# Performance work log

Hardware: AMD Instinct MI355X
Metric: run time of the kernel (lower is better)

## Reference

```python
import jax, jax.numpy as jnp
import numpy as np

V, D, T_MAX, H, L = 96, 128, 64, 8, 4
HD = D // H          # 16
FF = 4 * D           # 512
B, T = 4096, 64
EPS = 1e-5


def setup_inputs() -> dict:
    key = jax.random.key(0)
    ks = jax.random.split(key, 24)
    n = jax.random.normal
    inp = {
        'idx': jax.random.randint(ks[0], (B, T), 0, V),
        'targets': jax.random.randint(ks[1], (B, T), 0, V),
        'tok_emb': n(ks[2], (V, D), jnp.float32) * 0.02,
        'pos_emb': n(ks[3], (T_MAX, D), jnp.float32) * 0.02,
        # per-layer stacked params; weight layout follows torch Linear [out, in]
        'Wq': n(ks[4], (L, D, D), jnp.float32) * (1.0 / np.sqrt(D)),
        'Wk': n(ks[5], (L, D, D), jnp.float32) * (1.0 / np.sqrt(D)),
        'Wv': n(ks[6], (L, D, D), jnp.float32) * (1.0 / np.sqrt(D)),
        'Wo': n(ks[7], (L, D, D), jnp.float32) * (1.0 / np.sqrt(D)),
        'bo': jnp.zeros((L, D), jnp.float32),
        'ln1_g': jnp.ones((L, D), jnp.float32),
        'ln1_b': jnp.zeros((L, D), jnp.float32),
        'ln2_g': jnp.ones((L, D), jnp.float32),
        'ln2_b': jnp.zeros((L, D), jnp.float32),
        'W1': n(ks[8], (L, FF, D), jnp.float32) * (1.0 / np.sqrt(D)),
        'b1': jnp.zeros((L, FF), jnp.float32),
        'W2': n(ks[9], (L, D, FF), jnp.float32) * (1.0 / np.sqrt(FF)),
        'b2': jnp.zeros((L, D), jnp.float32),
        'lnf_g': jnp.ones((D,), jnp.float32),
        'lnf_b': jnp.zeros((D,), jnp.float32),
        'lm_b': jnp.zeros((V,), jnp.float32),
    }
    return inp


def _layernorm(x, g, b):
    mu = jnp.mean(x, axis=-1, keepdims=True)
    var = jnp.mean(jnp.square(x - mu), axis=-1, keepdims=True)
    return (x - mu) * jax.lax.rsqrt(var + EPS) * g + b


def reference(idx, targets, tok_emb, pos_emb, Wq, Wk, Wv, Wo, bo,
              ln1_g, ln1_b, ln2_g, ln2_b, W1, b1, W2, b2,
              lnf_g, lnf_b, lm_b):
    Bc, Tc = idx.shape
    x = tok_emb[idx] + pos_emb[:Tc]                      # [B,T,D]
    causal = jnp.tril(jnp.ones((Tc, Tc), bool))
    scale = HD ** -0.5
    for l in range(L):  # small fixed layer count
        xn = _layernorm(x, ln1_g[l], ln1_b[l])
        # per-head Linears are blocks of a single [D,D] matmul
        q = (xn @ Wq[l].T).reshape(Bc, Tc, H, HD)
        k = (xn @ Wk[l].T).reshape(Bc, Tc, H, HD)
        v = (xn @ Wv[l].T).reshape(Bc, Tc, H, HD)
        wei = jnp.einsum('bqhd,bkhd->bhqk', q, k) * scale
        wei = jnp.where(causal, wei, -jnp.inf)
        wei = jax.nn.softmax(wei, axis=-1)               # dropout = identity (eval)
        att = jnp.einsum('bhqk,bkhd->bqhd', wei, v).reshape(Bc, Tc, D)
        x = x + att @ Wo[l].T + bo[l]
        xn = _layernorm(x, ln2_g[l], ln2_b[l])
        h = jax.nn.gelu(xn @ W1[l].T + b1[l], approximate=False)
        x = x + h @ W2[l].T + b2[l]
    x = _layernorm(x, lnf_g, lnf_b)
    logits = x @ tok_emb.T + lm_b                        # tied weights
    logits = logits.reshape(Bc * Tc, V)
    logp = jax.nn.log_softmax(logits, axis=-1)
    loss = -jnp.mean(jnp.take_along_axis(logp, targets.reshape(-1, 1), axis=-1))
    return logits, loss
```

## Files before the change

### kernel.cpp

```cpp
#include <hip/hip_runtime.h>
#include <hip/hip_bf16.h>
#include <math.h>

#define PREP_THR 512

typedef __attribute__((ext_vector_type(8))) short bf16x8;
typedef __attribute__((ext_vector_type(4))) short bf16x4;
typedef __attribute__((ext_vector_type(4))) float f32x4;

#define MFMA32(a, b, c) __builtin_amdgcn_mfma_f32_16x16x32_bf16((a), (b), (c), 0, 0, 0)

#if defined(__has_builtin)
#if __has_builtin(__builtin_amdgcn_mfma_f32_16x16x16bf16_1k)
#define HAVE_MFMA16 1
#endif
#endif
#ifdef HAVE_MFMA16
#define MFMA16(a, b, c) __builtin_amdgcn_mfma_f32_16x16x16bf16_1k((a), (b), (c), 0, 0, 0)
#else
__device__ __forceinline__ f32x4 mfma16_fb(bf16x4 a, bf16x4 b, f32x4 c) {
  asm volatile("s_nop 1\n\tv_mfma_f32_16x16x16_bf16 %0, %1, %2, %0\n\ts_nop 7\n\ts_nop 7"
               : "+v"(c) : "v"(a), "v"(b));
  return c;
}
#define MFMA16(a, b, c) mfma16_fb((a), (b), (c))
#endif

#define WS_EMB 0
#define WS_WQ  12288
#define WS_WK  (WS_WQ + 65536)
#define WS_WV  (WS_WK + 65536)
#define WS_WO  (WS_WV + 65536)
#define WS_W1  (WS_WO + 65536)
#define WS_W2  (WS_W1 + 262144)
#define WS_END (WS_W2 + 262144)

__device__ __forceinline__ short f2bf(float f) {
  union { __hip_bfloat16 h; unsigned short s; } u;
  u.h = __float2bfloat16(f);
  return (short)u.s;
}
__device__ __forceinline__ bf16x4 pk4(f32x4 v) {
  bf16x4 r;
  r[0] = f2bf(v[0]); r[1] = f2bf(v[1]); r[2] = f2bf(v[2]); r[3] = f2bf(v[3]);
  return r;
}
__device__ __forceinline__ float gelu1(float x) {
  float y = x * __builtin_fmaf(0.0356774081f, x * x, 0.7978845608f);
  return x * __builtin_amdgcn_rcpf(1.f + exp2f(-2.885390082f * y));
}

__global__ void prep_weights(const float* __restrict__ tok_emb,
                             const float* __restrict__ Wq, const float* __restrict__ Wk,
                             const float* __restrict__ Wv, const float* __restrict__ Wo,
                             const float* __restrict__ W1, const float* __restrict__ W2,
                             short* __restrict__ wsb) {
  int i = blockIdx.x * PREP_THR + threadIdx.x;
  if (i < 12288) {
    int n = i >> 7, k = i & 127;
    wsb[WS_EMB + (k >> 3) * 768 + n * 8 + (k & 7)] = f2bf(tok_emb[i]);
    return;
  }
  i -= 12288;
  if (i < 262144) {
    int tensor = i >> 16;
    int rem = i & 65535;
    int l = rem >> 14;
    int w = rem & 16383;
    int n = w >> 7, k = w & 127;
    const float* src = tensor == 0 ? Wq : tensor == 1 ? Wk : tensor == 2 ? Wv : Wo;
    wsb[WS_WQ + tensor * 65536 + l * 16384 + (k >> 3) * 1024 + n * 8 + (k & 7)] =
        f2bf(src[rem]);
    return;
  }
  i -= 262144;
  if (i < 262144) {
    int l = i >> 16;
    int w = i & 65535;
    int n = w >> 7, k = w & 127;
    wsb[WS_W1 + l * 65536 + (k >> 3) * 4096 + n * 8 + (k & 7)] = f2bf(W1[i]);
    return;
  }
  i -= 262144;
  if (i < 262144) {
    int l = i >> 16;
    int w = i & 65535;
    int n = w >> 9, k = w & 511;
    wsb[WS_W2 + l * 65536 + (k >> 3) * 1024 + n * 8 + (k & 7)] = f2bf(W2[i]);
  }
}

__global__ __launch_bounds__(256, 2)
void lm_forward(const int* __restrict__ idx, const int* __restrict__ targets,
                const float* __restrict__ tok_emb, const float* __restrict__ pos_emb,
                const float* __restrict__ bo, const float* __restrict__ ln1_g,
                const float* __restrict__ ln1_b, const float* __restrict__ ln2_g,
                const float* __restrict__ ln2_b, const float* __restrict__ b1,
                const float* __restrict__ b2, const float* __restrict__ lnf_g,
                const float* __restrict__ lnf_b, const float* __restrict__ lm_b,
                const short* __restrict__ wsb, float* __restrict__ out,
                float* __restrict__ loss_part) {
  __shared__ __align__(16) short sXn[64 * 136];
  __shared__ __align__(16) char region[33792];
  __shared__ __align__(16) float sPart[4 * 64 * 2];
  __shared__ float sRed[64];
  short* sAtt = (short*)region;
  short* sH = (short*)region;
  float* sL = (float*)region;

  const int b = blockIdx.x;
  const int tid = threadIdx.x;
  const int wave = tid >> 6;
  const int lane = tid & 63;
  const int lr = lane & 15;
  const int lg = lane >> 4;
  const f32x4 fz = {0.f, 0.f, 0.f, 0.f};
  const float KSC = 0.360673760f;

  f32x4 x[2][4];
#pragma unroll
  for (int cg = 0; cg < 2; ++cg)
#pragma unroll
    for (int n = 0; n < 4; ++n) {
      int t = 16 * n + lr;
      int dim = wave * 32 + cg * 16 + lg * 4;
      int tk = idx[b * 64 + t];
      x[cg][n] = *(const f32x4*)(tok_emb + tk * 128 + dim) +
                 *(const f32x4*)(pos_emb + t * 128 + dim);
    }

  auto ln = [&](const float* g, const float* be) {
    float s[4], s2[4];
#pragma unroll
    for (int n = 0; n < 4; ++n) {
      float a = 0.f, a2 = 0.f;
#pragma unroll
      for (int cg = 0; cg < 2; ++cg)
#pragma unroll
        for (int r = 0; r < 4; ++r) {
          float v = x[cg][n][r];
          a += v; a2 += v * v;
        }
      s[n] = a; s2[n] = a2;
    }
#pragma unroll
    for (int n = 0; n < 4; ++n) {
      s[n] += __shfl_xor(s[n], 16, 64);  s[n] += __shfl_xor(s[n], 32, 64);
      s2[n] += __shfl_xor(s2[n], 16, 64); s2[n] += __shfl_xor(s2[n], 32, 64);
    }
    if (lg == 0) {
#pragma unroll
      for (int n = 0; n < 4; ++n) {
        float2 p; p.x = s[n]; p.y = s2[n];
        *(float2*)(sPart + (wave * 64 + 16 * n + lr) * 2) = p;
      }
    }
    __syncthreads();
    f32x4 g4[2], b4[2];
#pragma unroll
    for (int cg = 0; cg < 2; ++cg) {
      int dim = wave * 32 + cg * 16 + lg * 4;
      g4[cg] = *(const f32x4*)(g + dim);
      b4[cg] = *(const f32x4*)(be + dim);
    }
#pragma unroll
    for (int n = 0; n < 4; ++n) {
      float S = 0.f, S2 = 0.f;
#pragma unroll
      for (int w = 0; w < 4; ++w) {
        float2 p = *(const float2*)(sPart + (w * 64 + 16 * n + lr) * 2);
        S += p.x; S2 += p.y;
      }
      float mean = S * 0.0078125f;
      float rstd = rsqrtf(__builtin_fmaf(-mean, mean, S2 * 0.0078125f) + 1e-5f);
#pragma unroll
      for (int cg = 0; cg < 2; ++cg) {
        f32x4 o;
#pragma unroll
        for (int c = 0; c < 4; ++c)
          o[c] = __builtin_fmaf((x[cg][n][c] - mean) * rstd, g4[cg][c], b4[cg][c]);
        *(bf16x4*)(sXn + (16 * n + lr) * 136 + wave * 32 + cg * 16 + lg * 4) = pk4(o);
      }
    }
    __syncthreads();
  };

#pragma unroll 1
  for (int l = 0; l < 4; ++l) {
    ln(ln1_g + l * 128, ln1_b + l * 128);

    const short* wq = wsb + WS_WQ + l * 16384;
    const short* wk = wsb + WS_WK + l * 16384;
    const short* wv = wsb + WS_WV + l * 16384;
#pragma unroll
    for (int hs = 0; hs < 2; ++hs) {
      const int h = wave * 2 + hs;
      f32x4 aq[4], ak[4], av[4];
#pragma unroll
      for (int n = 0; n < 4; ++n) { aq[n] = fz; ak[n] = fz; av[n] = fz; }
#pragma unroll
      for (int ks = 0; ks < 4; ++ks) {
        bf16x8 xf[4];
#pragma unroll
        for (int n = 0; n < 4; ++n)
          xf[n] = *(const bf16x8*)(sXn + (16 * n + lr) * 136 + ks * 32 + lg * 8);
        int wo_ = (ks * 4 + lg) * 1024 + (h * 16 + lr) * 8;
        bf16x8 qw = *(const bf16x8*)(wq + wo_);
        bf16x8 kw = *(const bf16x8*)(wk + wo_);
        bf16x8 vw = *(const bf16x8*)(wv + wo_);
#pragma unroll
        for (int n = 0; n < 4; ++n) {
          aq[n] = MFMA32(qw, xf[n], aq[n]);
          ak[n] = MFMA32(kw, xf[n], ak[n]);
          av[n] = MFMA32(xf[n], vw, av[n]);
        }
      }
      bf16x4 qf[4], kf[4], vf[4];
#pragma unroll
      for (int n = 0; n < 4; ++n) {
        qf[n] = pk4(aq[n] * KSC);
        kf[n] = pk4(ak[n]);
        vf[n] = pk4(av[n]);
      }
      f32x4 sc[4][4];
#pragma unroll
      for (int n = 0; n < 4; ++n)
#pragma unroll
        for (int m = 0; m <= n; ++m)
          sc[m][n] = MFMA16(kf[m], qf[n], fz);
#pragma unroll
      for (int n = 0; n < 4; ++n) {
#pragma unroll
        for (int r = 0; r < 4; ++r)
          if (lg * 4 + r > lr) sc[n][n][r] = -1e30f;
        float mx = -1e30f;
#pragma unroll
        for (int m = 0; m <= n; ++m)
#pragma unroll
          for (int r = 0; r < 4; ++r) mx = fmaxf(mx, sc[m][n][r]);
        mx = fmaxf(mx, __shfl_xor(mx, 16, 64));
        mx = fmaxf(mx, __shfl_xor(mx, 32, 64));
        float sum = 0.f;
#pragma unroll
        for (int m = 0; m <= n; ++m)
#pragma unroll
          for (int r = 0; r < 4; ++r) {
            float p = exp2f(sc[m][n][r] - mx);
            sc[m][n][r] = p;
            sum += p;
          }
        sum += __shfl_xor(sum, 16, 64);
        sum += __shfl_xor(sum, 32, 64);
        float rinv = __builtin_amdgcn_rcpf(sum);
        f32x4 ao = fz;
#pragma unroll
        for (int m = 0; m <= n; ++m) {
          bf16x4 pf = pk4(sc[m][n] * rinv);
          ao = MFMA16(vf[m], pf, ao);
        }
        *(bf16x4*)(sAtt + (16 * n + lr) * 136 + h * 16 + lg * 4) = pk4(ao);
      }
    }
    __syncthreads();

    {
      const short* wo = wsb + WS_WO + l * 16384;
      f32x4 ac[2][4];
#pragma unroll
      for (int cg = 0; cg < 2; ++cg)
#pragma unroll
        for (int n = 0; n < 4; ++n) ac[cg][n] = fz;
#pragma unroll
      for (int ks = 0; ks < 4; ++ks) {
        bf16x8 af[4];
#pragma unroll
        for (int n = 0; n < 4; ++n)
          af[n] = *(const bf16x8*)(sAtt + (16 * n + lr) * 136 + ks * 32 + lg * 8);
#pragma unroll
        for (int cg = 0; cg < 2; ++cg) {
          bf16x8 wf = *(const bf16x8*)(wo + (ks * 4 + lg) * 1024 +
                                       (wave * 32 + cg * 16 + lr) * 8);
#pragma unroll
          for (int n = 0; n < 4; ++n) ac[cg][n] = MFMA32(wf, af[n], ac[cg][n]);
        }
      }
#pragma unroll
      for (int cg = 0; cg < 2; ++cg) {
        f32x4 bo4 = *(const f32x4*)(bo + l * 128 + wave * 32 + cg * 16 + lg * 4);
#pragma unroll
        for (int n = 0; n < 4; ++n) x[cg][n] = x[cg][n] + ac[cg][n] + bo4;
      }
    }

    ln(ln2_g + l * 128, ln2_b + l * 128);

    {
      const short* w1 = wsb + WS_W1 + l * 65536;
      const short* w2 = wsb + WS_W2 + l * 65536;
      f32x4 a2[2][4];
#pragma unroll
      for (int cg = 0; cg < 2; ++cg)
#pragma unroll
        for (int n = 0; n < 4; ++n) a2[cg][n] = fz;
#pragma unroll 1
      for (int c = 0; c < 2; ++c) {
        f32x4 a1[4][4];
#pragma unroll
        for (int g = 0; g < 4; ++g)
#pragma unroll
          for (int n = 0; n < 4; ++n) a1[g][n] = fz;
#pragma unroll
        for (int ks = 0; ks < 4; ++ks) {
          bf16x8 xf[4];
#pragma unroll
          for (int n = 0; n < 4; ++n)
            xf[n] = *(const bf16x8*)(sXn + (16 * n + lr) * 136 + ks * 32 + lg * 8);
#pragma unroll
          for (int g = 0; g < 4; ++g) {
            bf16x8 wf = *(const bf16x8*)(w1 + (ks * 4 + lg) * 4096 +
                                         (c * 256 + wave * 64 + g * 16 + lr) * 8);
#pragma unroll
            for (int n = 0; n < 4; ++n) a1[g][n] = MFMA32(wf, xf[n], a1[g][n]);
          }
        }
#pragma unroll
        for (int g = 0; g < 4; ++g) {
          f32x4 b1v = *(const f32x4*)(b1 + l * 512 + c * 256 + wave * 64 + g * 16 + lg * 4);
#pragma unroll
          for (int n = 0; n < 4; ++n) {
            f32x4 hv;
#pragma unroll
            for (int r = 0; r < 4; ++r) hv[r] = gelu1(a1[g][n][r] + b1v[r]);
            *(bf16x4*)(sH + (16 * n + lr) * 264 + wave * 64 + g * 16 + lg * 4) = pk4(hv);
          }
        }
        __syncthreads();
#pragma unroll
        for (int ks = 0; ks < 8; ++ks) {
          bf16x8 hf[4];
#pragma unroll
          for (int n = 0; n < 4; ++n)
            hf[n] = *(const bf16x8*)(sH + (16 * n + lr) * 264 + ks * 32 + lg * 8);
#pragma unroll
          for (int cg = 0; cg < 2; ++cg) {
            bf16x8 wf = *(const bf16x8*)(w2 + (c * 32 + ks * 4 + lg) * 1024 +
                                         (wave * 32 + cg * 16 + lr) * 8);
#pragma unroll
            for (int n = 0; n < 4; ++n) a2[cg][n] = MFMA32(wf, hf[n], a2[cg][n]);
          }
        }
        if (c == 0) __syncthreads();
      }
#pragma unroll
      for (int cg = 0; cg < 2; ++cg) {
        f32x4 b2v = *(const f32x4*)(b2 + l * 128 + wave * 32 + cg * 16 + lg * 4);
#pragma unroll
        for (int n = 0; n < 4; ++n) x[cg][n] = x[cg][n] + a2[cg][n] + b2v;
      }
    }
  }

  ln(lnf_g, lnf_b);

  {
    auto do_tile = [&](int vt) {
      f32x4 al[4];
#pragma unroll
      for (int n = 0; n < 4; ++n) al[n] = fz;
#pragma unroll
      for (int ks = 0; ks < 4; ++ks) {
        bf16x8 ef = *(const bf16x8*)(wsb + WS_EMB + (ks * 4 + lg) * 768 +
                                     (vt * 16 + lr) * 8);
#pragma unroll
        for (int n = 0; n < 4; ++n) {
          bf16x8 xf = *(const bf16x8*)(sXn + (16 * n + lr) * 136 + ks * 32 + lg * 8);
          al[n] = MFMA32(ef, xf, al[n]);
        }
      }
      f32x4 lb = *(const f32x4*)(lm_b + vt * 16 + lg * 4);
#pragma unroll
      for (int n = 0; n < 4; ++n) {
        f32x4 v = al[n] + lb;
        int t = 16 * n + lr;
        *(f32x4*)(out + ((size_t)b * 64 + t) * 96 + vt * 16 + lg * 4) = v;
        *(f32x4*)(sL + t * 100 + vt * 16 + lg * 4) = v;
      }
    };
    do_tile(wave);
    if (wave < 2) do_tile(wave + 4);
  }
  __syncthreads();

  {
    int r = tid >> 2, c4 = tid & 3;
    const float* lrow = sL + r * 100 + c4 * 24;
    float mx = -1e30f;
#pragma unroll
    for (int j = 0; j < 24; ++j) mx = fmaxf(mx, lrow[j]);
    mx = fmaxf(mx, __shfl_xor(mx, 1, 64));
    mx = fmaxf(mx, __shfl_xor(mx, 2, 64));
    float sum = 0.f;
#pragma unroll
    for (int j = 0; j < 24; ++j) sum += __expf(lrow[j] - mx);
    sum += __shfl_xor(sum, 1, 64);
    sum += __shfl_xor(sum, 2, 64);
    if (c4 == 0) {
      float lse = logf(sum) + mx;
      sRed[r] = lse - sL[r * 100 + targets[b * 64 + r]];
    }
  }
  __syncthreads();
  if (wave == 0) {
    float v = sRed[lane];
#pragma unroll
    for (int m = 32; m >= 1; m >>= 1) v += __shfl_xor(v, m, 64);
    if (lane == 0) loss_part[b] = v;
  }
}

__global__ void loss_reduce(const float* __restrict__ loss_part, float* __restrict__ out_loss) {
  __shared__ float red[256];
  int t = threadIdx.x;
  float s = 0.f;
  for (int i = t; i < 4096; i += 256) s += loss_part[i];
  red[t] = s;
  __syncthreads();
  for (int k = 128; k >= 1; k >>= 1) {
    if (t < k) red[t] += red[t + k];
    __syncthreads();
  }
  if (t == 0) out_loss[0] = red[0] * (1.f / 262144.f);
}

extern "C" void kernel_launch(void* const* d_in, const int* in_sizes, int n_in,
                              void* d_out, int out_size, void* d_ws, size_t ws_size,
                              hipStream_t stream) {
  (void)in_sizes; (void)n_in; (void)ws_size;
  const int* idx      = (const int*)d_in[0];
  const int* targets  = (const int*)d_in[1];
  const float* tok_emb = (const float*)d_in[2];
  const float* pos_emb = (const float*)d_in[3];
  const float* Wq = (const float*)d_in[4];
  const float* Wk = (const float*)d_in[5];
  const float* Wv = (const float*)d_in[6];
  const float* Wo = (const float*)d_in[7];
  const float* bo = (const float*)d_in[8];
  const float* ln1_g = (const float*)d_in[9];
  const float* ln1_b = (const float*)d_in[10];
  const float* ln2_g = (const float*)d_in[11];
  const float* ln2_b = (const float*)d_in[12];
  const float* W1 = (const float*)d_in[13];
  const float* b1 = (const float*)d_in[14];
  const float* W2 = (const float*)d_in[15];
  const float* b2 = (const float*)d_in[16];
  const float* lnf_g = (const float*)d_in[17];
  const float* lnf_b = (const float*)d_in[18];
  const float* lm_b = (const float*)d_in[19];

  short* wsb = (short*)d_ws;
  float* loss_part = (float*)((char*)d_ws + (size_t)WS_END * 2);
  float* out = (float*)d_out;

  prep_weights<<<1560, PREP_THR, 0, stream>>>(tok_emb, Wq, Wk, Wv, Wo, W1, W2, wsb);
  lm_forward<<<4096, 256, 0, stream>>>(idx, targets, tok_emb, pos_emb, bo,
                                       ln1_g, ln1_b, ln2_g, ln2_b, b1, b2,
                                       lnf_g, lnf_b, lm_b, wsb, out, loss_part);
  loss_reduce<<<1, 256, 0, stream>>>(loss_part, out + (out_size - 1));
}
```

Baseline: 869.4 us.

## Process two sequences per block to reuse weight fragments across sequences

Each block now handles two batch sequences with duplicated shared-memory buffers and register state, so every weight fragment loaded from global memory feeds MFMAs for both sequences. The Wo and W2 matmuls now accumulate directly into the residual registers instead of separate accumulators. Launch bounds drop to one block per CU-slot and the grid halves. This trades roughly double LDS and register use (lower occupancy, possible spills) for halved weight traffic and more MFMA work per load.

```diff
diff --git a/kernel.cpp b/kernel.cpp
--- a/kernel.cpp
+++ b/kernel.cpp
@@ -90,7 +90,7 @@
   }
 }
 
-__global__ __launch_bounds__(256, 2)
+__global__ __launch_bounds__(256, 1)
 void lm_forward(const int* __restrict__ idx, const int* __restrict__ targets,
                 const float* __restrict__ tok_emb, const float* __restrict__ pos_emb,
                 const float* __restrict__ bo, const float* __restrict__ ln1_g,
@@ -100,15 +100,12 @@
                 const float* __restrict__ lnf_b, const float* __restrict__ lm_b,
                 const short* __restrict__ wsb, float* __restrict__ out,
                 float* __restrict__ loss_part) {
-  __shared__ __align__(16) short sXn[64 * 136];
-  __shared__ __align__(16) char region[33792];
-  __shared__ __align__(16) float sPart[4 * 64 * 2];
-  __shared__ float sRed[64];
-  short* sAtt = (short*)region;
-  short* sH = (short*)region;
-  float* sL = (float*)region;
-
-  const int b = blockIdx.x;
+  __shared__ __align__(16) short sXn[2][64 * 136];
+  __shared__ __align__(16) char region[2][33792];
+  __shared__ __align__(16) float sPart[2][4 * 64 * 2];
+  __shared__ float sRed[2][64];
+
+  const int b0 = blockIdx.x * 2;
   const int tid = threadIdx.x;
   const int wave = tid >> 6;
   const int lane = tid & 63;
@@ -117,43 +114,53 @@
   const f32x4 fz = {0.f, 0.f, 0.f, 0.f};
   const float KSC = 0.360673760f;
 
-  f32x4 x[2][4];
-#pragma unroll
-  for (int cg = 0; cg < 2; ++cg)
-#pragma unroll
-    for (int n = 0; n < 4; ++n) {
-      int t = 16 * n + lr;
-      int dim = wave * 32 + cg * 16 + lg * 4;
-      int tk = idx[b * 64 + t];
-      x[cg][n] = *(const f32x4*)(tok_emb + tk * 128 + dim) +
-                 *(const f32x4*)(pos_emb + t * 128 + dim);
-    }
+  f32x4 x[2][2][4];
+#pragma unroll
+  for (int s = 0; s < 2; ++s)
+#pragma unroll
+    for (int cg = 0; cg < 2; ++cg)
+#pragma unroll
+      for (int n = 0; n < 4; ++n) {
+        int t = 16 * n + lr;
+        int dim = wave * 32 + cg * 16 + lg * 4;
+        int tk = idx[(b0 + s) * 64 + t];
+        x[s][cg][n] = *(const f32x4*)(tok_emb + tk * 128 + dim) +
+                      *(const f32x4*)(pos_emb + t * 128 + dim);
+      }
 
   auto ln = [&](const float* g, const float* be) {
-    float s[4], s2[4];
-#pragma unroll
-    for (int n = 0; n < 4; ++n) {
-      float a = 0.f, a2 = 0.f;
-#pragma unroll
-      for (int cg = 0; cg < 2; ++cg)
-#pragma unroll
-        for (int r = 0; r < 4; ++r) {
-          float v = x[cg][n][r];
-          a += v; a2 += v * v;
-        }
-      s[n] = a; s2[n] = a2;
-    }
-#pragma unroll
-    for (int n = 0; n < 4; ++n) {
-      s[n] += __shfl_xor(s[n], 16, 64);  s[n] += __shfl_xor(s[n], 32, 64);
-      s2[n] += __shfl_xor(s2[n], 16, 64); s2[n] += __shfl_xor(s2[n], 32, 64);
-    }
+    float S1[2][4], S2[2][4];
+#pragma unroll
+    for (int s = 0; s < 2; ++s)
+#pragma unroll
+      for (int n = 0; n < 4; ++n) {
+        float a = 0.f, a2 = 0.f;
+#pragma unroll
+        for (int cg = 0; cg < 2; ++cg)
+#pragma unroll
+          for (int r = 0; r < 4; ++r) {
+            float v = x[s][cg][n][r];
+            a += v; a2 += v * v;
+          }
+        S1[s][n] = a; S2[s][n] = a2;
+      }
+#pragma unroll
+    for (int s = 0; s < 2; ++s)
+#pragma unroll
+      for (int n = 0; n < 4; ++n) {
+        S1[s][n] += __shfl_xor(S1[s][n], 16, 64);
+        S1[s][n] += __shfl_xor(S1[s][n], 32, 64);
+        S2[s][n] += __shfl_xor(S2[s][n], 16, 64);
+        S2[s][n] += __shfl_xor(S2[s][n], 32, 64);
+      }
     if (lg == 0) {
 #pragma unroll
-      for (int n = 0; n < 4; ++n) {
-        float2 p; p.x = s[n]; p.y = s2[n];
-        *(float2*)(sPart + (wave * 64 + 16 * n + lr) * 2) = p;
-      }
+      for (int s = 0; s < 2; ++s)
+#pragma unroll
+        for (int n = 0; n < 4; ++n) {
+          float2 p; p.x = S1[s][n]; p.y = S2[s][n];
+          *(float2*)(sPart[s] + (wave * 64 + 16 * n + lr) * 2) = p;
+        }
     }
     __syncthreads();
     f32x4 g4[2], b4[2];
@@ -164,24 +171,26 @@
       b4[cg] = *(const f32x4*)(be + dim);
     }
 #pragma unroll
-    for (int n = 0; n < 4; ++n) {
-      float S = 0.f, S2 = 0.f;
-#pragma unroll
-      for (int w = 0; w < 4; ++w) {
-        float2 p = *(const float2*)(sPart + (w * 64 + 16 * n + lr) * 2);
-        S += p.x; S2 += p.y;
-      }
-      float mean = S * 0.0078125f;
-      float rstd = rsqrtf(__builtin_fmaf(-mean, mean, S2 * 0.0078125f) + 1e-5f);
-#pragma unroll
-      for (int cg = 0; cg < 2; ++cg) {
-        f32x4 o;
-#pragma unroll
-        for (int c = 0; c < 4; ++c)
-          o[c] = __builtin_fmaf((x[cg][n][c] - mean) * rstd, g4[cg][c], b4[cg][c]);
-        *(bf16x4*)(sXn + (16 * n + lr) * 136 + wave * 32 + cg * 16 + lg * 4) = pk4(o);
-      }
-    }
+    for (int s = 0; s < 2; ++s)
+#pragma unroll
+      for (int n = 0; n < 4; ++n) {
+        float S = 0.f, Q = 0.f;
+#pragma unroll
+        for (int w = 0; w < 4; ++w) {
+          float2 p = *(const float2*)(sPart[s] + (w * 64 + 16 * n + lr) * 2);
+          S += p.x; Q += p.y;
+        }
+        float mean = S * 0.0078125f;
+        float rstd = rsqrtf(__builtin_fmaf(-mean, mean, Q * 0.0078125f) + 1e-5f);
+#pragma unroll
+        for (int cg = 0; cg < 2; ++cg) {
+          f32x4 o;
+#pragma unroll
+          for (int c = 0; c < 4; ++c)
+            o[c] = __builtin_fmaf((x[s][cg][n][c] - mean) * rstd, g4[cg][c], b4[cg][c]);
+          *(bf16x4*)(sXn[s] + (16 * n + lr) * 136 + wave * 32 + cg * 16 + lg * 4) = pk4(o);
+        }
+      }
     __syncthreads();
   };
 
@@ -192,103 +201,109 @@
     const short* wq = wsb + WS_WQ + l * 16384;
     const short* wk = wsb + WS_WK + l * 16384;
     const short* wv = wsb + WS_WV + l * 16384;
-#pragma unroll
+#pragma unroll 1
     for (int hs = 0; hs < 2; ++hs) {
       const int h = wave * 2 + hs;
-      f32x4 aq[4], ak[4], av[4];
-#pragma unroll
-      for (int n = 0; n < 4; ++n) { aq[n] = fz; ak[n] = fz; av[n] = fz; }
+      f32x4 aq[2][4], ak[2][4], av[2][4];
+#pragma unroll
+      for (int s = 0; s < 2; ++s)
+#pragma unroll
+        for (int n = 0; n < 4; ++n) { aq[s][n] = fz; ak[s][n] = fz; av[s][n] = fz; }
 #pragma unroll
       for (int ks = 0; ks < 4; ++ks) {
-        bf16x8 xf[4];
-#pragma unroll
-        for (int n = 0; n < 4; ++n)
-          xf[n] = *(const bf16x8*)(sXn + (16 * n + lr) * 136 + ks * 32 + lg * 8);
         int wo_ = (ks * 4 + lg) * 1024 + (h * 16 + lr) * 8;
         bf16x8 qw = *(const bf16x8*)(wq + wo_);
         bf16x8 kw = *(const bf16x8*)(wk + wo_);
         bf16x8 vw = *(const bf16x8*)(wv + wo_);
 #pragma unroll
+        for (int s = 0; s < 2; ++s)
+#pragma unroll
+          for (int n = 0; n < 4; ++n) {
+            bf16x8 xf = *(const bf16x8*)(sXn[s] + (16 * n + lr) * 136 + ks * 32 + lg * 8);
+            aq[s][n] = MFMA32(qw, xf, aq[s][n]);
+            ak[s][n] = MFMA32(kw, xf, ak[s][n]);
+            av[s][n] = MFMA32(xf, vw, av[s][n]);
+          }
+      }
+#pragma unroll
+      for (int s = 0; s < 2; ++s) {
+        bf16x4 qf[4], kf[4], vf[4];
+#pragma unroll
         for (int n = 0; n < 4; ++n) {
-          aq[n] = MFMA32(qw, xf[n], aq[n]);
-          ak[n] = MFMA32(kw, xf[n], ak[n]);
-          av[n] = MFMA32(xf[n], vw, av[n]);
-        }
-      }
-      bf16x4 qf[4], kf[4], vf[4];
-#pragma unroll
-      for (int n = 0; n < 4; ++n) {
-        qf[n] = pk4(aq[n] * KSC);
-        kf[n] = pk4(ak[n]);
-        vf[n] = pk4(av[n]);
-      }
-      f32x4 sc[4][4];
-#pragma unroll
-      for (int n = 0; n < 4; ++n)
-#pragma unroll
-        for (int m = 0; m <= n; ++m)
-          sc[m][n] = MFMA16(kf[m], qf[n], fz);
-#pragma unroll
-      for (int n = 0; n < 4; ++n) {
-#pragma unroll
-        for (int r = 0; r < 4; ++r)
-          if (lg * 4 + r > lr) sc[n][n][r] = -1e30f;
-        float mx = -1e30f;
-#pragma unroll
-        for (int m = 0; m <= n; ++m)
-#pragma unroll
-          for (int r = 0; r < 4; ++r) mx = fmaxf(mx, sc[m][n][r]);
-        mx = fmaxf(mx, __shfl_xor(mx, 16, 64));
-        mx = fmaxf(mx, __shfl_xor(mx, 32, 64));
-        float sum = 0.f;
-#pragma unroll
-        for (int m = 0; m <= n; ++m)
-#pragma unroll
-          for (int r = 0; r < 4; ++r) {
-            float p = exp2f(sc[m][n][r] - mx);
-            sc[m][n][r] = p;
-            sum += p;
+          qf[n] = pk4(aq[s][n] * KSC);
+          kf[n] = pk4(ak[s][n]);
+          vf[n] = pk4(av[s][n]);
+        }
+        f32x4 sc[4][4];
+#pragma unroll
+        for (int n = 0; n < 4; ++n)
+#pragma unroll
+          for (int m = 0; m <= n; ++m)
+            sc[m][n] = MFMA16(kf[m], qf[n], fz);
+        short* sAtt = (short*)region[s];
+#pragma unroll
+        for (int n = 0; n < 4; ++n) {
+#pragma unroll
+          for (int r = 0; r < 4; ++r)
+            if (lg * 4 + r > lr) sc[n][n][r] = -1e30f;
+          float mx = -1e30f;
+#pragma unroll
+          for (int m = 0; m <= n; ++m)
+#pragma unroll
+            for (int r = 0; r < 4; ++r) mx = fmaxf(mx, sc[m][n][r]);
+          mx = fmaxf(mx, __shfl_xor(mx, 16, 64));
+          mx = fmaxf(mx, __shfl_xor(mx, 32, 64));
+          float sum = 0.f;
+#pragma unroll
+          for (int m = 0; m <= n; ++m)
+#pragma unroll
+            for (int r = 0; r < 4; ++r) {
+              float p = exp2f(sc[m][n][r] - mx);
+              sc[m][n][r] = p;
+              sum += p;
+            }
+          sum += __shfl_xor(sum, 16, 64);
+          sum += __shfl_xor(sum, 32, 64);
+          float rinv = __builtin_amdgcn_rcpf(sum);
+          f32x4 ao = fz;
+#pragma unroll
+          for (int m = 0; m <= n; ++m) {
+            bf16x4 pf = pk4(sc[m][n] * rinv);
+            ao = MFMA16(vf[m], pf, ao);
           }
-        sum += __shfl_xor(sum, 16, 64);
-        sum += __shfl_xor(sum, 32, 64);
-        float rinv = __builtin_amdgcn_rcpf(sum);
-        f32x4 ao = fz;
-#pragma unroll
-        for (int m = 0; m <= n; ++m) {
-          bf16x4 pf = pk4(sc[m][n] * rinv);
-          ao = MFMA16(vf[m], pf, ao);
-        }
-        *(bf16x4*)(sAtt + (16 * n + lr) * 136 + h * 16 + lg * 4) = pk4(ao);
+          *(bf16x4*)(sAtt + (16 * n + lr) * 136 + h * 16 + lg * 4) = pk4(ao);
+        }
       }
     }
     __syncthreads();
 
     {
       const short* wo = wsb + WS_WO + l * 16384;
-      f32x4 ac[2][4];
-#pragma unroll
-      for (int cg = 0; cg < 2; ++cg)
-#pragma unroll
-        for (int n = 0; n < 4; ++n) ac[cg][n] = fz;
 #pragma unroll
       for (int ks = 0; ks < 4; ++ks) {
-        bf16x8 af[4];
-#pragma unroll
-        for (int n = 0; n < 4; ++n)
-          af[n] = *(const bf16x8*)(sAtt + (16 * n + lr) * 136 + ks * 32 + lg * 8);
-#pragma unroll
-        for (int cg = 0; cg < 2; ++cg) {
-          bf16x8 wf = *(const bf16x8*)(wo + (ks * 4 + lg) * 1024 +
-                                       (wave * 32 + cg * 16 + lr) * 8);
-#pragma unroll
-          for (int n = 0; n < 4; ++n) ac[cg][n] = MFMA32(wf, af[n], ac[cg][n]);
-        }
+        bf16x8 wf[2];
+#pragma unroll
+        for (int cg = 0; cg < 2; ++cg)
+          wf[cg] = *(const bf16x8*)(wo + (ks * 4 + lg) * 1024 +
+                                    (wave * 32 + cg * 16 + lr) * 8);
+#pragma unroll
+        for (int s = 0; s < 2; ++s)
+#pragma unroll
+          for (int n = 0; n < 4; ++n) {
+            bf16x8 af = *(const bf16x8*)((short*)region[s] +
+                                         (16 * n + lr) * 136 + ks * 32 + lg * 8);
+#pragma unroll
+            for (int cg = 0; cg < 2; ++cg)
+              x[s][cg][n] = MFMA32(wf[cg], af, x[s][cg][n]);
+          }
       }
 #pragma unroll
       for (int cg = 0; cg < 2; ++cg) {
         f32x4 bo4 = *(const f32x4*)(bo + l * 128 + wave * 32 + cg * 16 + lg * 4);
 #pragma unroll
-        for (int n = 0; n < 4; ++n) x[cg][n] = x[cg][n] + ac[cg][n] + bo4;
+        for (int s = 0; s < 2; ++s)
+#pragma unroll
+          for (int n = 0; n < 4; ++n) x[s][cg][n] = x[s][cg][n] + bo4;
       }
     }
 
@@ -297,57 +312,63 @@
     {
       const short* w1 = wsb + WS_W1 + l * 65536;
       const short* w2 = wsb + WS_W2 + l * 65536;
-      f32x4 a2[2][4];
-#pragma unroll
-      for (int cg = 0; cg < 2; ++cg)
-#pragma unroll
-        for (int n = 0; n < 4; ++n) a2[cg][n] = fz;
 #pragma unroll 1
       for (int c = 0; c < 2; ++c) {
-        f32x4 a1[4][4];
-#pragma unroll
-        for (int g = 0; g < 4; ++g)
-#pragma unroll
-          for (int n = 0; n < 4; ++n) a1[g][n] = fz;
+        f32x4 a1[2][4][4];
+#pragma unroll
+        for (int s = 0; s < 2; ++s)
+#pragma unroll
+          for (int g = 0; g < 4; ++g)
+#pragma unroll
+            for (int n = 0; n < 4; ++n) a1[s][g][n] = fz;
 #pragma unroll
         for (int ks = 0; ks < 4; ++ks) {
-          bf16x8 xf[4];
-#pragma unroll
-          for (int n = 0; n < 4; ++n)
-            xf[n] = *(const bf16x8*)(sXn + (16 * n + lr) * 136 + ks * 32 + lg * 8);
-#pragma unroll
-          for (int g = 0; g < 4; ++g) {
-            bf16x8 wf = *(const bf16x8*)(w1 + (ks * 4 + lg) * 4096 +
-                                         (c * 256 + wave * 64 + g * 16 + lr) * 8);
-#pragma unroll
-            for (int n = 0; n < 4; ++n) a1[g][n] = MFMA32(wf, xf[n], a1[g][n]);
-          }
+          bf16x8 wf[4];
+#pragma unroll
+          for (int g = 0; g < 4; ++g)
+            wf[g] = *(const bf16x8*)(w1 + (ks * 4 + lg) * 4096 +
+                                     (c * 256 + wave * 64 + g * 16 + lr) * 8);
+#pragma unroll
+          for (int s = 0; s < 2; ++s)
+#pragma unroll
+            for (int n = 0; n < 4; ++n) {
+              bf16x8 xf = *(const bf16x8*)(sXn[s] + (16 * n + lr) * 136 + ks * 32 + lg * 8);
+#pragma unroll
+              for (int g = 0; g < 4; ++g) a1[s][g][n] = MFMA32(wf[g], xf, a1[s][g][n]);
+            }
         }
 #pragma unroll
         for (int g = 0; g < 4; ++g) {
           f32x4 b1v = *(const f32x4*)(b1 + l * 512 + c * 256 + wave * 64 + g * 16 + lg * 4);
 #pragma unroll
-          for (int n = 0; n < 4; ++n) {
-            f32x4 hv;
-#pragma unroll
-            for (int r = 0; r < 4; ++r) hv[r] = gelu1(a1[g][n][r] + b1v[r]);
-            *(bf16x4*)(sH + (16 * n + lr) * 264 + wave * 64 + g * 16 + lg * 4) = pk4(hv);
-          }
+          for (int s = 0; s < 2; ++s)
+#pragma unroll
+            for (int n = 0; n < 4; ++n) {
+              f32x4 hv;
+#pragma unroll
+              for (int r = 0; r < 4; ++r) hv[r] = gelu1(a1[s][g][n][r] + b1v[r]);
+              *(bf16x4*)((short*)region[s] + (16 * n + lr) * 264 +
+                         wave * 64 + g * 16 + lg * 4) = pk4(hv);
+            }
         }
         __syncthreads();
 #pragma unroll
         for (int ks = 0; ks < 8; ++ks) {
-          bf16x8 hf[4];
-#pragma unroll
-          for (int n = 0; n < 4; ++n)
-            hf[n] = *(const bf16x8*)(sH + (16 * n + lr) * 264 + ks * 32 + lg * 8);
-#pragma unroll
-          for (int cg = 0; cg < 2; ++cg) {
-            bf16x8 wf = *(const bf16x8*)(w2 + (c * 32 + ks * 4 + lg) * 1024 +
-                                         (wave * 32 + cg * 16 + lr) * 8);
-#pragma unroll
-            for (int n = 0; n < 4; ++n) a2[cg][n] = MFMA32(wf, hf[n], a2[cg][n]);
-          }
+          bf16x8 wf[2];
+#pragma unroll
+          for (int cg = 0; cg < 2; ++cg)
+            wf[cg] = *(const bf16x8*)(w2 + (c * 32 + ks * 4 + lg) * 1024 +
+                                      (wave * 32 + cg * 16 + lr) * 8);
+#pragma unroll
+          for (int s = 0; s < 2; ++s)
+#pragma unroll
+            for (int n = 0; n < 4; ++n) {
+              bf16x8 hf = *(const bf16x8*)((short*)region[s] +
+                                           (16 * n + lr) * 264 + ks * 32 + lg * 8);
+#pragma unroll
+              for (int cg = 0; cg < 2; ++cg)
+                x[s][cg][n] = MFMA32(wf[cg], hf, x[s][cg][n]);
+            }
         }
         if (c == 0) __syncthreads();
       }
@@ -355,7 +376,9 @@
       for (int cg = 0; cg < 2; ++cg) {
         f32x4 b2v = *(const f32x4*)(b2 + l * 128 + wave * 32 + cg * 16 + lg * 4);
 #pragma unroll
-        for (int n = 0; n < 4; ++n) x[cg][n] = x[cg][n] + a2[cg][n] + b2v;
+        for (int s = 0; s < 2; ++s)
+#pragma unroll
+          for (int n = 0; n < 4; ++n) x[s][cg][n] = x[s][cg][n] + b2v;
       }
     }
   }
@@ -363,7 +386,7 @@
   ln(lnf_g, lnf_b);
 
   {
-    auto do_tile = [&](int vt) {
+    auto do_tile = [&](int s, int vt) {
       f32x4 al[4];
 #pragma unroll
       for (int n = 0; n < 4; ++n) al[n] = fz;
@@ -373,48 +396,56 @@
                                      (vt * 16 + lr) * 8);
 #pragma unroll
         for (int n = 0; n < 4; ++n) {
-          bf16x8 xf = *(const bf16x8*)(sXn + (16 * n + lr) * 136 + ks * 32 + lg * 8);
+          bf16x8 xf = *(const bf16x8*)(sXn[s] + (16 * n + lr) * 136 + ks * 32 + lg * 8);
           al[n] = MFMA32(ef, xf, al[n]);
         }
       }
       f32x4 lb = *(const f32x4*)(lm_b + vt * 16 + lg * 4);
+      float* sL = (float*)region[s];
 #pragma unroll
       for (int n = 0; n < 4; ++n) {
         f32x4 v = al[n] + lb;
         int t = 16 * n + lr;
-        *(f32x4*)(out + ((size_t)b * 64 + t) * 96 + vt * 16 + lg * 4) = v;
+        *(f32x4*)(out + ((size_t)(b0 + s) * 64 + t) * 96 + vt * 16 + lg * 4) = v;
         *(f32x4*)(sL + t * 100 + vt * 16 + lg * 4) = v;
       }
     };
-    do_tile(wave);
-    if (wave < 2) do_tile(wave + 4);
+#pragma unroll
+    for (int s = 0; s < 2; ++s) {
+      do_tile(s, wave);
+      if (wave < 2) do_tile(s, wave + 4);
+    }
   }
   __syncthreads();
 
   {
     int r = tid >> 2, c4 = tid & 3;
-    const float* lrow = sL + r * 100 + c4 * 24;
-    float mx = -1e30f;
-#pragma unroll
-    for (int j = 0; j < 24; ++j) mx = fmaxf(mx, lrow[j]);
-    mx = fmaxf(mx, __shfl_xor(mx, 1, 64));
-    mx = fmaxf(mx, __shfl_xor(mx, 2, 64));
-    float sum = 0.f;
-#pragma unroll
-    for (int j = 0; j < 24; ++j) sum += __expf(lrow[j] - mx);
-    sum += __shfl_xor(sum, 1, 64);
-    sum += __shfl_xor(sum, 2, 64);
-    if (c4 == 0) {
-      float lse = logf(sum) + mx;
-      sRed[r] = lse - sL[r * 100 + targets[b * 64 + r]];
+#pragma unroll
+    for (int s = 0; s < 2; ++s) {
+      const float* sL = (const float*)region[s];
+      const float* lrow = sL + r * 100 + c4 * 24;
+      float mx = -1e30f;
+#pragma unroll
+      for (int j = 0; j < 24; ++j) mx = fmaxf(mx, lrow[j]);
+      mx = fmaxf(mx, __shfl_xor(mx, 1, 64));
+      mx = fmaxf(mx, __shfl_xor(mx, 2, 64));
+      float sum = 0.f;
+#pragma unroll
+      for (int j = 0; j < 24; ++j) sum += __expf(lrow[j] - mx);
+      sum += __shfl_xor(sum, 1, 64);
+      sum += __shfl_xor(sum, 2, 64);
+      if (c4 == 0) {
+        float lse = logf(sum) + mx;
+        sRed[s][r] = lse - sL[r * 100 + targets[(b0 + s) * 64 + r]];
+      }
     }
   }
   __syncthreads();
-  if (wave == 0) {
-    float v = sRed[lane];
+  if (wave < 2) {
+    float v = sRed[wave][lane];
 #pragma unroll
     for (int m = 32; m >= 1; m >>= 1) v += __shfl_xor(v, m, 64);
-    if (lane == 0) loss_part[b] = v;
+    if (lane == 0) loss_part[b0 + wave] = v;
   }
 }
 
@@ -462,7 +493,7 @@
   float* out = (float*)d_out;
 
   prep_weights<<<1560, PREP_THR, 0, stream>>>(tok_emb, Wq, Wk, Wv, Wo, W1, W2, wsb);
-  lm_forward<<<4096, 256, 0, stream>>>(idx, targets, tok_emb, pos_emb, bo,
+  lm_forward<<<2048, 256, 0, stream>>>(idx, targets, tok_emb, pos_emb, bo,
                                        ln1_g, ln1_b, ln2_g, ln2_b, b1, b2,
                                        lnf_g, lnf_b, lm_b, wsb, out, loss_part);
   loss_reduce<<<1, 256, 0, stream>>>(loss_part, out + (out_size - 1));
```

After: 1.256 ms. 1.44x slower.

## Repartition work so each wave owns 16 token rows across all dims

Applied to the files above, without the earlier changes.

Switches the per-block split from waves owning 32 feature columns to waves owning 16 token rows. LayerNorm becomes wave-local, the residual stays in MFMA accumulators, and the MLP hidden chunks and the logits/loss stay in the wave's own rows, which removes most block barriers. Attention now goes through K and V written to shared memory and needs one barrier before use. Each wave loads every weight tile for Q/K/V/O/W1/W2, which increases weight traffic per block, and causal attention work is unbalanced across waves since later waves do up to four key tiles.

```diff
diff --git a/kernel.cpp b/kernel.cpp
--- a/kernel.cpp
+++ b/kernel.cpp
@@ -101,316 +101,280 @@
                 const short* __restrict__ wsb, float* __restrict__ out,
                 float* __restrict__ loss_part) {
   __shared__ __align__(16) short sXn[64 * 136];
-  __shared__ __align__(16) char region[33792];
-  __shared__ __align__(16) float sPart[4 * 64 * 2];
+  __shared__ __align__(16) char regionB[36864];
   __shared__ float sRed[64];
-  short* sAtt = (short*)region;
-  short* sH = (short*)region;
-  float* sL = (float*)region;
+  short* sKT = (short*)regionB;
+  short* sVT = (short*)(regionB + 17408);
+  short* sAw = (short*)regionB;
+  short* sH  = (short*)(regionB + 18432);
 
   const int b = blockIdx.x;
   const int tid = threadIdx.x;
-  const int wave = tid >> 6;
+  const int w = tid >> 6;
   const int lane = tid & 63;
   const int lr = lane & 15;
   const int lg = lane >> 4;
+  const int myrow = w * 16 + lr;
   const f32x4 fz = {0.f, 0.f, 0.f, 0.f};
   const float KSC = 0.360673760f;
 
-  f32x4 x[2][4];
-#pragma unroll
-  for (int cg = 0; cg < 2; ++cg)
-#pragma unroll
-    for (int n = 0; n < 4; ++n) {
-      int t = 16 * n + lr;
-      int dim = wave * 32 + cg * 16 + lg * 4;
-      int tk = idx[b * 64 + t];
-      x[cg][n] = *(const f32x4*)(tok_emb + tk * 128 + dim) +
-                 *(const f32x4*)(pos_emb + t * 128 + dim);
-    }
+  f32x4 x[8];
+  {
+    int tk = idx[b * 64 + myrow];
+#pragma unroll
+    for (int t = 0; t < 8; ++t) {
+      int dim = t * 16 + lg * 4;
+      x[t] = *(const f32x4*)(tok_emb + tk * 128 + dim) +
+             *(const f32x4*)(pos_emb + myrow * 128 + dim);
+    }
+  }
 
   auto ln = [&](const float* g, const float* be) {
-    float s[4], s2[4];
-#pragma unroll
-    for (int n = 0; n < 4; ++n) {
-      float a = 0.f, a2 = 0.f;
-#pragma unroll
-      for (int cg = 0; cg < 2; ++cg)
-#pragma unroll
-        for (int r = 0; r < 4; ++r) {
-          float v = x[cg][n][r];
-          a += v; a2 += v * v;
-        }
-      s[n] = a; s2[n] = a2;
-    }
-#pragma unroll
-    for (int n = 0; n < 4; ++n) {
-      s[n] += __shfl_xor(s[n], 16, 64);  s[n] += __shfl_xor(s[n], 32, 64);
-      s2[n] += __shfl_xor(s2[n], 16, 64); s2[n] += __shfl_xor(s2[n], 32, 64);
-    }
-    if (lg == 0) {
-#pragma unroll
-      for (int n = 0; n < 4; ++n) {
-        float2 p; p.x = s[n]; p.y = s2[n];
-        *(float2*)(sPart + (wave * 64 + 16 * n + lr) * 2) = p;
-      }
-    }
-    __syncthreads();
-    f32x4 g4[2], b4[2];
-#pragma unroll
-    for (int cg = 0; cg < 2; ++cg) {
-      int dim = wave * 32 + cg * 16 + lg * 4;
-      g4[cg] = *(const f32x4*)(g + dim);
-      b4[cg] = *(const f32x4*)(be + dim);
-    }
-#pragma unroll
-    for (int n = 0; n < 4; ++n) {
-      float S = 0.f, S2 = 0.f;
-#pragma unroll
-      for (int w = 0; w < 4; ++w) {
-        float2 p = *(const float2*)(sPart + (w * 64 + 16 * n + lr) * 2);
-        S += p.x; S2 += p.y;
-      }
-      float mean = S * 0.0078125f;
-      float rstd = rsqrtf(__builtin_fmaf(-mean, mean, S2 * 0.0078125f) + 1e-5f);
-#pragma unroll
-      for (int cg = 0; cg < 2; ++cg) {
-        f32x4 o;
-#pragma unroll
-        for (int c = 0; c < 4; ++c)
-          o[c] = __builtin_fmaf((x[cg][n][c] - mean) * rstd, g4[cg][c], b4[cg][c]);
-        *(bf16x4*)(sXn + (16 * n + lr) * 136 + wave * 32 + cg * 16 + lg * 4) = pk4(o);
-      }
-    }
-    __syncthreads();
+    float s = 0.f, s2 = 0.f;
+#pragma unroll
+    for (int t = 0; t < 8; ++t)
+#pragma unroll
+      for (int r = 0; r < 4; ++r) { float v = x[t][r]; s += v; s2 += v * v; }
+    s += __shfl_xor(s, 16, 64);  s += __shfl_xor(s, 32, 64);
+    s2 += __shfl_xor(s2, 16, 64); s2 += __shfl_xor(s2, 32, 64);
+    float mean = s * 0.0078125f;
+    float rstd = rsqrtf(__builtin_fmaf(-mean, mean, s2 * 0.0078125f) + 1e-5f);
+#pragma unroll
+    for (int t = 0; t < 8; ++t) {
+      int dim = t * 16 + lg * 4;
+      f32x4 g4 = *(const f32x4*)(g + dim);
+      f32x4 b4 = *(const f32x4*)(be + dim);
+      f32x4 o;
+#pragma unroll
+      for (int c = 0; c < 4; ++c)
+        o[c] = __builtin_fmaf((x[t][c] - mean) * rstd, g4[c], b4[c]);
+      *(bf16x4*)(sXn + myrow * 136 + dim) = pk4(o);
+    }
+  };
+  auto load_xb = [&](bf16x8* xb) {
+#pragma unroll
+    for (int ks = 0; ks < 4; ++ks)
+      xb[ks] = *(const bf16x8*)(sXn + myrow * 136 + ks * 32 + lg * 8);
   };
 
 #pragma unroll 1
   for (int l = 0; l < 4; ++l) {
     ln(ln1_g + l * 128, ln1_b + l * 128);
+    bf16x8 xb[4];
+    load_xb(xb);
 
     const short* wq = wsb + WS_WQ + l * 16384;
     const short* wk = wsb + WS_WK + l * 16384;
     const short* wv = wsb + WS_WV + l * 16384;
-#pragma unroll
-    for (int hs = 0; hs < 2; ++hs) {
-      const int h = wave * 2 + hs;
-      f32x4 aq[4], ak[4], av[4];
-#pragma unroll
-      for (int n = 0; n < 4; ++n) { aq[n] = fz; ak[n] = fz; av[n] = fz; }
-#pragma unroll
-      for (int ks = 0; ks < 4; ++ks) {
-        bf16x8 xf[4];
-#pragma unroll
-        for (int n = 0; n < 4; ++n)
-          xf[n] = *(const bf16x8*)(sXn + (16 * n + lr) * 136 + ks * 32 + lg * 8);
-        int wo_ = (ks * 4 + lg) * 1024 + (h * 16 + lr) * 8;
-        bf16x8 qw = *(const bf16x8*)(wq + wo_);
-        bf16x8 kw = *(const bf16x8*)(wk + wo_);
-        bf16x8 vw = *(const bf16x8*)(wv + wo_);
-#pragma unroll
-        for (int n = 0; n < 4; ++n) {
-          aq[n] = MFMA32(qw, xf[n], aq[n]);
-          ak[n] = MFMA32(kw, xf[n], ak[n]);
-          av[n] = MFMA32(xf[n], vw, av[n]);
-        }
-      }
-      bf16x4 qf[4], kf[4], vf[4];
-#pragma unroll
-      for (int n = 0; n < 4; ++n) {
-        qf[n] = pk4(aq[n] * KSC);
-        kf[n] = pk4(ak[n]);
-        vf[n] = pk4(av[n]);
-      }
-      f32x4 sc[4][4];
-#pragma unroll
-      for (int n = 0; n < 4; ++n)
-#pragma unroll
-        for (int m = 0; m <= n; ++m)
-          sc[m][n] = MFMA16(kf[m], qf[n], fz);
-#pragma unroll
-      for (int n = 0; n < 4; ++n) {
-#pragma unroll
-        for (int r = 0; r < 4; ++r)
-          if (lg * 4 + r > lr) sc[n][n][r] = -1e30f;
-        float mx = -1e30f;
-#pragma unroll
-        for (int m = 0; m <= n; ++m)
-#pragma unroll
-          for (int r = 0; r < 4; ++r) mx = fmaxf(mx, sc[m][n][r]);
-        mx = fmaxf(mx, __shfl_xor(mx, 16, 64));
-        mx = fmaxf(mx, __shfl_xor(mx, 32, 64));
-        float sum = 0.f;
-#pragma unroll
-        for (int m = 0; m <= n; ++m)
+
+    bf16x4 qf[8];
+    {
+      f32x4 aq[8];
+#pragma unroll
+      for (int h = 0; h < 8; ++h) aq[h] = fz;
+#pragma unroll
+      for (int ks = 0; ks < 4; ++ks)
+#pragma unroll
+        for (int h = 0; h < 8; ++h) {
+          bf16x8 wf = *(const bf16x8*)(wq + (ks * 4 + lg) * 1024 + (h * 16 + lr) * 8);
+          aq[h] = MFMA32(wf, xb[ks], aq[h]);
+        }
+#pragma unroll
+      for (int h = 0; h < 8; ++h) qf[h] = pk4(aq[h] * KSC);
+    }
+    {
+      f32x4 ak[8];
+#pragma unroll
+      for (int h = 0; h < 8; ++h) ak[h] = fz;
+#pragma unroll
+      for (int ks = 0; ks < 4; ++ks)
+#pragma unroll
+        for (int h = 0; h < 8; ++h) {
+          bf16x8 wf = *(const bf16x8*)(wk + (ks * 4 + lg) * 1024 + (h * 16 + lr) * 8);
+          ak[h] = MFMA32(wf, xb[ks], ak[h]);
+        }
+#pragma unroll
+      for (int h = 0; h < 8; ++h)
+        *(bf16x4*)(sKT + myrow * 136 + h * 16 + lg * 4) = pk4(ak[h]);
+    }
+    {
+      f32x4 av[8];
+#pragma unroll
+      for (int h = 0; h < 8; ++h) av[h] = fz;
+#pragma unroll
+      for (int ks = 0; ks < 4; ++ks)
+#pragma unroll
+        for (int h = 0; h < 8; ++h) {
+          bf16x8 wf = *(const bf16x8*)(wv + (ks * 4 + lg) * 1024 + (h * 16 + lr) * 8);
+          av[h] = MFMA32(xb[ks], wf, av[h]);
+        }
+#pragma unroll
+      for (int h = 0; h < 8; ++h)
+        *(bf16x4*)(sVT + (h * 16 + lr) * 76 + w * 16 + lg * 4) = pk4(av[h]);
+    }
+    __syncthreads();
+
+    bf16x4 ab[8];
+#pragma unroll 1
+    for (int h = 0; h < 8; ++h) {
+      f32x4 sc[4];
+#pragma unroll
+      for (int m = 0; m < 4; ++m)
+        if (m <= w) {
+          bf16x4 kfr = *(const bf16x4*)(sKT + (m * 16 + lr) * 136 + h * 16 + lg * 4);
+          sc[m] = MFMA16(kfr, qf[h], fz);
+          if (m == w) {
+#pragma unroll
+            for (int r = 0; r < 4; ++r)
+              if (lg * 4 + r > lr) sc[m][r] = -1e30f;
+          }
+        }
+      float mx = -1e30f;
+#pragma unroll
+      for (int m = 0; m < 4; ++m)
+        if (m <= w)
+#pragma unroll
+          for (int r = 0; r < 4; ++r) mx = fmaxf(mx, sc[m][r]);
+      mx = fmaxf(mx, __shfl_xor(mx, 16, 64));
+      mx = fmaxf(mx, __shfl_xor(mx, 32, 64));
+      float sum = 0.f;
+#pragma unroll
+      for (int m = 0; m < 4; ++m)
+        if (m <= w)
 #pragma unroll
           for (int r = 0; r < 4; ++r) {
-            float p = exp2f(sc[m][n][r] - mx);
-            sc[m][n][r] = p;
+            float p = exp2f(sc[m][r] - mx);
+            sc[m][r] = p;
             sum += p;
           }
-        sum += __shfl_xor(sum, 16, 64);
-        sum += __shfl_xor(sum, 32, 64);
-        float rinv = __builtin_amdgcn_rcpf(sum);
-        f32x4 ao = fz;
-#pragma unroll
-        for (int m = 0; m <= n; ++m) {
-          bf16x4 pf = pk4(sc[m][n] * rinv);
-          ao = MFMA16(vf[m], pf, ao);
-        }
-        *(bf16x4*)(sAtt + (16 * n + lr) * 136 + h * 16 + lg * 4) = pk4(ao);
-      }
+      sum += __shfl_xor(sum, 16, 64);
+      sum += __shfl_xor(sum, 32, 64);
+      float rinv = __builtin_amdgcn_rcpf(sum);
+      f32x4 ao = fz;
+#pragma unroll
+      for (int m = 0; m < 4; ++m)
+        if (m <= w) {
+          bf16x4 vfr = *(const bf16x4*)(sVT + (h * 16 + lr) * 76 + m * 16 + lg * 4);
+          bf16x4 pf = pk4(sc[m] * rinv);
+          ao = MFMA16(vfr, pf, ao);
+        }
+      ab[h] = pk4(ao);
     }
     __syncthreads();
 
     {
+#pragma unroll
+      for (int h = 0; h < 8; ++h)
+        *(bf16x4*)(sAw + myrow * 136 + h * 16 + lg * 4) = ab[h];
+      bf16x8 atb[4];
+#pragma unroll
+      for (int ks = 0; ks < 4; ++ks)
+        atb[ks] = *(const bf16x8*)(sAw + myrow * 136 + ks * 32 + lg * 8);
       const short* wo = wsb + WS_WO + l * 16384;
-      f32x4 ac[2][4];
-#pragma unroll
-      for (int cg = 0; cg < 2; ++cg)
-#pragma unroll
-        for (int n = 0; n < 4; ++n) ac[cg][n] = fz;
-#pragma unroll
-      for (int ks = 0; ks < 4; ++ks) {
-        bf16x8 af[4];
-#pragma unroll
-        for (int n = 0; n < 4; ++n)
-          af[n] = *(const bf16x8*)(sAtt + (16 * n + lr) * 136 + ks * 32 + lg * 8);
-#pragma unroll
-        for (int cg = 0; cg < 2; ++cg) {
-          bf16x8 wf = *(const bf16x8*)(wo + (ks * 4 + lg) * 1024 +
-                                       (wave * 32 + cg * 16 + lr) * 8);
-#pragma unroll
-          for (int n = 0; n < 4; ++n) ac[cg][n] = MFMA32(wf, af[n], ac[cg][n]);
-        }
-      }
-#pragma unroll
-      for (int cg = 0; cg < 2; ++cg) {
-        f32x4 bo4 = *(const f32x4*)(bo + l * 128 + wave * 32 + cg * 16 + lg * 4);
-#pragma unroll
-        for (int n = 0; n < 4; ++n) x[cg][n] = x[cg][n] + ac[cg][n] + bo4;
-      }
+#pragma unroll
+      for (int ks = 0; ks < 4; ++ks)
+#pragma unroll
+        for (int t = 0; t < 8; ++t) {
+          bf16x8 wf = *(const bf16x8*)(wo + (ks * 4 + lg) * 1024 + (t * 16 + lr) * 8);
+          x[t] = MFMA32(wf, atb[ks], x[t]);
+        }
+#pragma unroll
+      for (int t = 0; t < 8; ++t)
+        x[t] = x[t] + *(const f32x4*)(bo + l * 128 + t * 16 + lg * 4);
     }
 
     ln(ln2_g + l * 128, ln2_b + l * 128);
+    load_xb(xb);
 
     {
       const short* w1 = wsb + WS_W1 + l * 65536;
       const short* w2 = wsb + WS_W2 + l * 65536;
-      f32x4 a2[2][4];
-#pragma unroll
-      for (int cg = 0; cg < 2; ++cg)
-#pragma unroll
-        for (int n = 0; n < 4; ++n) a2[cg][n] = fz;
 #pragma unroll 1
-      for (int c = 0; c < 2; ++c) {
-        f32x4 a1[4][4];
-#pragma unroll
-        for (int g = 0; g < 4; ++g)
-#pragma unroll
-          for (int n = 0; n < 4; ++n) a1[g][n] = fz;
-#pragma unroll
-        for (int ks = 0; ks < 4; ++ks) {
-          bf16x8 xf[4];
-#pragma unroll
-          for (int n = 0; n < 4; ++n)
-            xf[n] = *(const bf16x8*)(sXn + (16 * n + lr) * 136 + ks * 32 + lg * 8);
-#pragma unroll
-          for (int g = 0; g < 4; ++g) {
+      for (int c = 0; c < 4; ++c) {
+        f32x4 a1[8];
+#pragma unroll
+        for (int t2 = 0; t2 < 8; ++t2) a1[t2] = fz;
+#pragma unroll
+        for (int ks = 0; ks < 4; ++ks)
+#pragma unroll
+          for (int t2 = 0; t2 < 8; ++t2) {
             bf16x8 wf = *(const bf16x8*)(w1 + (ks * 4 + lg) * 4096 +
-                                         (c * 256 + wave * 64 + g * 16 + lr) * 8);
-#pragma unroll
-            for (int n = 0; n < 4; ++n) a1[g][n] = MFMA32(wf, xf[n], a1[g][n]);
+                                         (c * 128 + t2 * 16 + lr) * 8);
+            a1[t2] = MFMA32(wf, xb[ks], a1[t2]);
           }
-        }
-#pragma unroll
-        for (int g = 0; g < 4; ++g) {
-          f32x4 b1v = *(const f32x4*)(b1 + l * 512 + c * 256 + wave * 64 + g * 16 + lg * 4);
-#pragma unroll
-          for (int n = 0; n < 4; ++n) {
-            f32x4 hv;
-#pragma unroll
-            for (int r = 0; r < 4; ++r) hv[r] = gelu1(a1[g][n][r] + b1v[r]);
-            *(bf16x4*)(sH + (16 * n + lr) * 264 + wave * 64 + g * 16 + lg * 4) = pk4(hv);
+#pragma unroll
+        for (int t2 = 0; t2 < 8; ++t2) {
+          int hd = c * 128 + t2 * 16 + lg * 4;
+          f32x4 b1v = *(const f32x4*)(b1 + l * 512 + hd);
+          f32x4 hv;
+#pragma unroll
+          for (int r = 0; r < 4; ++r) hv[r] = gelu1(a1[t2][r] + b1v[r]);
+          *(bf16x4*)(sH + myrow * 136 + t2 * 16 + lg * 4) = pk4(hv);
+        }
+        bf16x8 hb[4];
+#pragma unroll
+        for (int ks = 0; ks < 4; ++ks)
+          hb[ks] = *(const bf16x8*)(sH + myrow * 136 + ks * 32 + lg * 8);
+#pragma unroll
+        for (int ks = 0; ks < 4; ++ks)
+#pragma unroll
+          for (int t = 0; t < 8; ++t) {
+            bf16x8 wf = *(const bf16x8*)(w2 + (c * 16 + ks * 4 + lg) * 1024 +
+                                         (t * 16 + lr) * 8);
+            x[t] = MFMA32(wf, hb[ks], x[t]);
           }
-        }
-        __syncthreads();
-#pragma unroll
-        for (int ks = 0; ks < 8; ++ks) {
-          bf16x8 hf[4];
-#pragma unroll
-          for (int n = 0; n < 4; ++n)
-            hf[n] = *(const bf16x8*)(sH + (16 * n + lr) * 264 + ks * 32 + lg * 8);
-#pragma unroll
-          for (int cg = 0; cg < 2; ++cg) {
-            bf16x8 wf = *(const bf16x8*)(w2 + (c * 32 + ks * 4 + lg) * 1024 +
-                                         (wave * 32 + cg * 16 + lr) * 8);
-#pragma unroll
-            for (int n = 0; n < 4; ++n) a2[cg][n] = MFMA32(wf, hf[n], a2[cg][n]);
-          }
-        }
-        if (c == 0) __syncthreads();
       }
 #pragma unroll
-      for (int cg = 0; cg < 2; ++cg) {
-        f32x4 b2v = *(const f32x4*)(b2 + l * 128 + wave * 32 + cg * 16 + lg * 4);
-#pragma unroll
-        for (int n = 0; n < 4; ++n) x[cg][n] = x[cg][n] + a2[cg][n] + b2v;
-      }
-    }
+      for (int t = 0; t < 8; ++t)
+        x[t] = x[t] + *(const f32x4*)(b2 + l * 128 + t * 16 + lg * 4);
+    }
+    __syncthreads();
   }
 
   ln(lnf_g, lnf_b);
-
   {
-    auto do_tile = [&](int vt) {
-      f32x4 al[4];
-#pragma unroll
-      for (int n = 0; n < 4; ++n) al[n] = fz;
-#pragma unroll
-      for (int ks = 0; ks < 4; ++ks) {
+    bf16x8 xb[4];
+    load_xb(xb);
+    f32x4 al[6];
+#pragma unroll
+    for (int vt = 0; vt < 6; ++vt) al[vt] = fz;
+#pragma unroll
+    for (int ks = 0; ks < 4; ++ks)
+#pragma unroll
+      for (int vt = 0; vt < 6; ++vt) {
         bf16x8 ef = *(const bf16x8*)(wsb + WS_EMB + (ks * 4 + lg) * 768 +
                                      (vt * 16 + lr) * 8);
-#pragma unroll
-        for (int n = 0; n < 4; ++n) {
-          bf16x8 xf = *(const bf16x8*)(sXn + (16 * n + lr) * 136 + ks * 32 + lg * 8);
-          al[n] = MFMA32(ef, xf, al[n]);
-        }
+        al[vt] = MFMA32(ef, xb[ks], al[vt]);
       }
+    int cgt = targets[b * 64 + myrow];
+    float mx = -1e30f, tsel = 0.f;
+#pragma unroll
+    for (int vt = 0; vt < 6; ++vt) {
       f32x4 lb = *(const f32x4*)(lm_b + vt * 16 + lg * 4);
-#pragma unroll
-      for (int n = 0; n < 4; ++n) {
-        f32x4 v = al[n] + lb;
-        int t = 16 * n + lr;
-        *(f32x4*)(out + ((size_t)b * 64 + t) * 96 + vt * 16 + lg * 4) = v;
-        *(f32x4*)(sL + t * 100 + vt * 16 + lg * 4) = v;
+      al[vt] = al[vt] + lb;
+      *(f32x4*)(out + ((size_t)b * 64 + myrow) * 96 + vt * 16 + lg * 4) = al[vt];
+#pragma unroll
+      for (int r = 0; r < 4; ++r) {
+        mx = fmaxf(mx, al[vt][r]);
+        if ((cgt >> 4) == vt && ((cgt >> 2) & 3) == lg && (cgt & 3) == r)
+          tsel = al[vt][r];
       }
-    };
-    do_tile(wave);
-    if (wave < 2) do_tile(wave + 4);
+    }
+    mx = fmaxf(mx, __shfl_xor(mx, 16, 64));
+    mx = fmaxf(mx, __shfl_xor(mx, 32, 64));
+    float sum = 0.f;
+#pragma unroll
+    for (int vt = 0; vt < 6; ++vt)
+#pragma unroll
+      for (int r = 0; r < 4; ++r) sum += __expf(al[vt][r] - mx);
+    sum += __shfl_xor(sum, 16, 64);
+    sum += __shfl_xor(sum, 32, 64);
+    tsel += __shfl_xor(tsel, 16, 64);
+    tsel += __shfl_xor(tsel, 32, 64);
+    if (lg == 0) sRed[myrow] = mx + logf(sum) - tsel;
   }
   __syncthreads();
-
-  {
-    int r = tid >> 2, c4 = tid & 3;
-    const float* lrow = sL + r * 100 + c4 * 24;
-    float mx = -1e30f;
-#pragma unroll
-    for (int j = 0; j < 24; ++j) mx = fmaxf(mx, lrow[j]);
-    mx = fmaxf(mx, __shfl_xor(mx, 1, 64));
-    mx = fmaxf(mx, __shfl_xor(mx, 2, 64));
-    float sum = 0.f;
-#pragma unroll
-    for (int j = 0; j < 24; ++j) sum += __expf(lrow[j] - mx);
-    sum += __shfl_xor(sum, 1, 64);
-    sum += __shfl_xor(sum, 2, 64);
-    if (c4 == 0) {
-      float lse = logf(sum) + mx;
-      sRed[r] = lse - sL[r * 100 + targets[b * 64 + r]];
-    }
-  }
-  __syncthreads();
-  if (wave == 0) {
+  if (w == 0) {
     float v = sRed[lane];
 #pragma unroll
     for (int m = 32; m >= 1; m >>= 1) v += __shfl_xor(v, m, 64);
```

New measurement: 3.446 ms. 3.96x slower.
